# Performance work log

Hardware: AMD Instinct MI355X
Metric: run time of the kernel (lower is better)

The kernel has to match this reference:

```python
import jax, jax.numpy as jnp
import numpy as np


def setup_inputs() -> dict:
    key = jax.random.key(0)
    k1, k2, k3 = jax.random.split(key, 3)
    shape = (2, 16, 2048, 64)  # (b, num_heads, seq_len, d_k)
    Q = jax.random.normal(k1, shape, dtype=jnp.float32)
    K = jax.random.normal(k2, shape, dtype=jnp.float32)
    V = jax.random.normal(k3, shape, dtype=jnp.float32)
    return {"Q": Q, "K": K, "V": V}


def reference(Q, K, V):
    # Mathematically identical to the blockwise online-softmax loop:
    # causal softmax attention with scale 1/sqrt(d_k), plus logsumexp L.
    d_k = Q.shape[-1]
    seq_len = Q.shape[2]
    scale = 1.0 / np.sqrt(d_k).astype(np.float32)
    # scores: [b, h, q, k]
    S = jnp.einsum("bhqd,bhkd->bhqk", Q, K) * scale
    causal_mask = jnp.tril(jnp.ones((seq_len, seq_len), dtype=bool))  # k_pos <= q_pos
    S = jnp.where(causal_mask, S, -jnp.inf)
    # L_i = m_i + log(l_i) == logsumexp over key dim (every row has >=1 valid key)
    L = jax.nn.logsumexp(S, axis=-1, keepdims=True)  # [b, h, q, 1]
    P = jnp.exp(S - L)  # normalized probabilities (deferred-normalization result)
    O = jnp.einsum("bhqk,bhkd->bhqd", P, V)
    return O, L
```

## Files before the change

### kernel.cpp

```cpp
#include <hip/hip_runtime.h>
#include <hip/hip_bf16.h>

#define S_LEN 2048
#define DH    64
#define NBH   32
#define KSCALE 0.1803368801111f
#define LN2    0.6931471805599453f
#define MB2    4.0f

typedef short v4s __attribute__((ext_vector_type(4)));
typedef short v8s __attribute__((ext_vector_type(8)));
typedef float v4f __attribute__((ext_vector_type(4)));

__device__ __forceinline__ unsigned short f2bf(float f){
  union { float f; unsigned int u; } v; v.f = f;
  return (unsigned short)((v.u + 0x7FFFu + ((v.u >> 16) & 1u)) >> 16);
}

__device__ __forceinline__ void gld16(void* lds, const void* g){
  __builtin_amdgcn_global_load_lds(
      (const __attribute__((address_space(1))) unsigned int*)g,
      (__attribute__((address_space(3))) unsigned int*)lds, 16, 0, 0);
}

__global__ __launch_bounds__(256) void prep(const float* __restrict__ K,
                                            const float* __restrict__ V,
                                            unsigned short* __restrict__ Kf,
                                            unsigned short* __restrict__ Vf){
  __shared__ unsigned short s[64 * 72];
  const int t   = blockIdx.x;
  const int bh  = blockIdx.y;
  const int tid = threadIdx.x;

  const float* Ksrc = K + ((size_t)bh * S_LEN + t * 64) * DH;
  #pragma unroll
  for (int i = 0; i < 4; ++i){
    int f = tid + i * 256;
    float4 v = ((const float4*)Ksrc)[f];
    int row = f >> 4, col = (f & 15) * 4;
    ushort4 o; o.x = f2bf(v.x); o.y = f2bf(v.y); o.z = f2bf(v.z); o.w = f2bf(v.w);
    *(ushort4*)(&s[row * 72 + col]) = o;
  }
  __syncthreads();
  unsigned short* KfT = Kf + ((size_t)bh * 32 + t) * 4096;
  #pragma unroll
  for (int i = 0; i < 2; ++i){
    int item = tid + i * 256;
    int c = item >> 6, l = item & 63;
    int kb = c >> 1, h = c & 1;
    v8s frag = *(const v8s*)(&s[(kb * 16 + (l & 15)) * 72 + h * 32 + (l >> 4) * 8]);
    *(v8s*)(&KfT[c * 512 + l * 8]) = frag;
  }
  __syncthreads();

  const float* Vsrc = V + ((size_t)bh * S_LEN + t * 64) * DH;
  #pragma unroll
  for (int i = 0; i < 4; ++i){
    int f = tid + i * 256;
    float4 v = ((const float4*)Vsrc)[f];
    int k = f >> 4, d = (f & 15) * 4;
    s[(d + 0) * 72 + k] = f2bf(v.x);
    s[(d + 1) * 72 + k] = f2bf(v.y);
    s[(d + 2) * 72 + k] = f2bf(v.z);
    s[(d + 3) * 72 + k] = f2bf(v.w);
  }
  __syncthreads();
  unsigned short* VfT = Vf + ((size_t)bh * 32 + t) * 4096;
  #pragma unroll
  for (int i = 0; i < 2; ++i){
    int item = tid + i * 256;
    int c = item >> 6, l = item & 63;
    int db = c >> 1, kp = c & 1;
    int dd = db * 16 + (l & 15);
    int kk = kp * 32 + (l >> 4) * 4;
    v4s a = *(const v4s*)(&s[dd * 72 + kk]);
    v4s b = *(const v4s*)(&s[dd * 72 + kk + 16]);
    v8s fr; fr[0]=a[0]; fr[1]=a[1]; fr[2]=a[2]; fr[3]=a[3];
            fr[4]=b[0]; fr[5]=b[1]; fr[6]=b[2]; fr[7]=b[3];
    *(v8s*)(&VfT[c * 512 + l * 8]) = fr;
  }
}

__global__ __launch_bounds__(256, 3) void fa_fwd(
    const float* __restrict__ Q,
    const unsigned short* __restrict__ Kf,
    const unsigned short* __restrict__ Vf,
    float* __restrict__ O, float* __restrict__ L)
{
  __shared__ __align__(16) char smem[2][16384];

  const int tid  = threadIdx.x;
  const int w    = tid >> 6;
  const int lane = tid & 63;
  const int lq   = lane & 15;
  const int g    = lane >> 4;
  const int bid  = blockIdx.x;
  const int qt   = 31 - (bid >> 5);
  const int bh   = bid & 31;
  const int M    = qt + 1;

  const unsigned short* KfB = Kf + (size_t)bh * 32 * 4096;
  const unsigned short* VfB = Vf + (size_t)bh * 32 * 4096;

  auto issue = [&](int t, char* buf){
    #pragma unroll
    for (int i = 0; i < 2; ++i){
      const int slot = tid + i * 256;
      gld16(buf        + slot * 16, KfB + (size_t)t * 4096 + slot * 8);
      gld16(buf + 8192 + slot * 16, VfB + (size_t)t * 4096 + slot * 8);
    }
  };

  v8s qf[4][2];
  #pragma unroll
  for (int s = 0; s < 4; ++s){
    const float* qp = Q + (size_t)(bh * S_LEN + qt * 64 + s * 16 + lq) * DH + g * 8;
    #pragma unroll
    for (int h = 0; h < 2; ++h){
      float4 a = *(const float4*)(qp + h * 32);
      float4 b = *(const float4*)(qp + h * 32 + 4);
      v8s qv;
      qv[0]=(short)f2bf(a.x*KSCALE); qv[1]=(short)f2bf(a.y*KSCALE);
      qv[2]=(short)f2bf(a.z*KSCALE); qv[3]=(short)f2bf(a.w*KSCALE);
      qv[4]=(short)f2bf(b.x*KSCALE); qv[5]=(short)f2bf(b.y*KSCALE);
      qv[6]=(short)f2bf(b.z*KSCALE); qv[7]=(short)f2bf(b.w*KSCALE);
      qf[s][h] = qv;
    }
  }

  issue(0, smem[0]);

  const v4f zero  = {0.f, 0.f, 0.f, 0.f};
  const v4f minit = {-MB2, -MB2, -MB2, -MB2};
  v4f acc[4][4];
  #pragma unroll
  for (int s = 0; s < 4; ++s)
    #pragma unroll
    for (int db = 0; db < 4; ++db) acc[s][db] = zero;
  float l4[4] = {0.f, 0.f, 0.f, 0.f};

  const int kb    = w;
  const int koff0 = (kb * 2    ) * 1024 + lane * 16;
  const int koff1 = (kb * 2 + 1) * 1024 + lane * 16;
  const int vsub  = (kb >> 1) * 1024 + (kb & 1) * 8 + lane * 16;

  for (int t = 0; t < M; ++t){
    const int tn = (t + 1 < M) ? t + 1 : t;
    issue(tn, smem[(t + 1) & 1]);
    asm volatile("s_waitcnt vmcnt(4)" ::: "memory");
    __builtin_amdgcn_s_barrier();
    __builtin_amdgcn_sched_barrier(0);

    const char* kbase = smem[t & 1];
    const char* vbase = smem[t & 1] + 8192;

    v8s kf0 = *(const v8s*)(kbase + koff0);
    v8s kf1 = *(const v8s*)(kbase + koff1);
    v4s vv[4];
    #pragma unroll
    for (int db = 0; db < 4; ++db)
      vv[db] = *(const v4s*)(vbase + db * 2048 + vsub);

    float p4[4][4];
    __builtin_amdgcn_s_setprio(1);
    #pragma unroll
    for (int s = 0; s < 4; ++s){
      v4f st = minit;
      st = __builtin_amdgcn_mfma_f32_16x16x32_bf16(kf0, qf[s][0], st, 0, 0, 0);
      st = __builtin_amdgcn_mfma_f32_16x16x32_bf16(kf1, qf[s][1], st, 0, 0, 0);
      p4[s][0] = st[0]; p4[s][1] = st[1]; p4[s][2] = st[2]; p4[s][3] = st[3];
    }
    __builtin_amdgcn_s_setprio(0);

    if (t == qt){
      #pragma unroll
      for (int s = 0; s < 4; ++s)
        #pragma unroll
        for (int r = 0; r < 4; ++r)
          if (kb * 16 + g * 4 + r > s * 16 + lq) p4[s][r] = -INFINITY;
    }

    v4s pf[4];
    #pragma unroll
    for (int s = 0; s < 4; ++s){
      #pragma unroll
      for (int r = 0; r < 4; ++r){
        const float pe = __builtin_amdgcn_exp2f(p4[s][r]);
        p4[s][r] = pe;
        l4[s] += pe;
      }
      unsigned u0, u1;
      asm("v_cvt_pk_bf16_f32 %0, %1, %2" : "=v"(u0) : "v"(p4[s][0]), "v"(p4[s][1]));
      asm("v_cvt_pk_bf16_f32 %0, %1, %2" : "=v"(u1) : "v"(p4[s][2]), "v"(p4[s][3]));
      union { unsigned u[2]; v4s s4; } P; P.u[0] = u0; P.u[1] = u1;
      pf[s] = P.s4;
    }

    __builtin_amdgcn_s_setprio(1);
    #pragma unroll
    for (int s = 0; s < 4; ++s){
      acc[s][0] = __builtin_amdgcn_mfma_f32_16x16x16bf16_1k(vv[0], pf[s], acc[s][0], 0, 0, 0);
      acc[s][1] = __builtin_amdgcn_mfma_f32_16x16x16bf16_1k(vv[1], pf[s], acc[s][1], 0, 0, 0);
      acc[s][2] = __builtin_amdgcn_mfma_f32_16x16x16bf16_1k(vv[2], pf[s], acc[s][2], 0, 0, 0);
      acc[s][3] = __builtin_amdgcn_mfma_f32_16x16x16bf16_1k(vv[3], pf[s], acc[s][3], 0, 0, 0);
    }
    __builtin_amdgcn_s_setprio(0);
    __builtin_amdgcn_s_barrier();
    __builtin_amdgcn_sched_barrier(0);
  }

  asm volatile("s_waitcnt vmcnt(0)" ::: "memory");
  __builtin_amdgcn_sched_barrier(0);
  __syncthreads();

  #pragma unroll
  for (int s = 0; s < 4; ++s){
    l4[s] += __shfl_xor(l4[s], 16);
    l4[s] += __shfl_xor(l4[s], 32);
  }
  float* Lr = (float*)smem[1];
  if (lane < 16){
    #pragma unroll
    for (int s = 0; s < 4; ++s) Lr[(w * 4 + s) * 16 + lane] = l4[s];
  }
  __syncthreads();
  const float lfw = Lr[(0 * 4 + w) * 16 + lq] + Lr[(1 * 4 + w) * 16 + lq]
                  + Lr[(2 * 4 + w) * 16 + lq] + Lr[(3 * 4 + w) * 16 + lq];
  const float invw = 1.f / lfw;

  v4f* Or = (v4f*)smem[0];
  float* Ob = O + ((size_t)bh * S_LEN + qt * 64 + w * 16 + lq) * DH;
  #pragma unroll
  for (int db = 0; db < 4; ++db){
    __syncthreads();
    #pragma unroll
    for (int s = 0; s < 4; ++s) Or[((w * 4 + s) * 16 + lq) * 4 + g] = acc[s][db];
    __syncthreads();
    v4f o = Or[((0 * 4 + w) * 16 + lq) * 4 + g] + Or[((1 * 4 + w) * 16 + lq) * 4 + g]
          + Or[((2 * 4 + w) * 16 + lq) * 4 + g] + Or[((3 * 4 + w) * 16 + lq) * 4 + g];
    o *= invw;
    *(v4f*)(Ob + db * 16 + g * 4) = o;
  }
  if (lane < 16)
    L[(size_t)bh * S_LEN + qt * 64 + w * 16 + lane] = logf(lfw) + MB2 * LN2;
}

__global__ __launch_bounds__(64) void fa_naive(
    const float* __restrict__ Q, const float* __restrict__ K,
    const float* __restrict__ V, float* __restrict__ O, float* __restrict__ L)
{
  const int q  = blockIdx.x;
  const int bh = blockIdx.y;
  const int d  = threadIdx.x;
  const float qv = Q[(size_t)(bh * S_LEN + q) * DH + d];
  float m = -INFINITY, l = 0.f, o = 0.f;
  for (int k = 0; k <= q; ++k){
    float s = qv * K[(size_t)(bh * S_LEN + k) * DH + d];
    #pragma unroll
    for (int off = 32; off > 0; off >>= 1) s += __shfl_xor(s, off);
    s *= 0.125f;
    const float mn = fmaxf(m, s);
    const float sfc = expf(m - mn);
    const float pe = expf(s - mn);
    l = l * sfc + pe;
    o = o * sfc + pe * V[(size_t)(bh * S_LEN + k) * DH + d];
    m = mn;
  }
  O[(size_t)(bh * S_LEN + q) * DH + d] = o / l;
  if (d == 0) L[(size_t)bh * S_LEN + q] = m + logf(l);
}

extern "C" void kernel_launch(void* const* d_in, const int* in_sizes, int n_in,
                              void* d_out, int out_size, void* d_ws, size_t ws_size,
                              hipStream_t stream)
{
  (void)in_sizes; (void)n_in; (void)out_size;
  const float* Q = (const float*)d_in[0];
  const float* K = (const float*)d_in[1];
  const float* V = (const float*)d_in[2];
  float* O = (float*)d_out;
  float* L = O + (size_t)NBH * S_LEN * DH;

  const size_t half = (size_t)NBH * S_LEN * DH * sizeof(unsigned short);
  if (ws_size >= 2 * half){
    unsigned short* Kf = (unsigned short*)d_ws;
    unsigned short* Vf = Kf + (size_t)NBH * S_LEN * DH;
    prep<<<dim3(S_LEN / 64, NBH), 256, 0, stream>>>(K, V, Kf, Vf);
    fa_fwd<<<dim3(1024), 256, 0, stream>>>(Q, Kf, Vf, O, L);
  } else {
    fa_naive<<<dim3(S_LEN, NBH), 64, 0, stream>>>(Q, K, V, O, L);
  }
}
```

Measured before the change: 48.82 us.

## Repack V fragments for 16-byte LDS reads, reorder tiles, raise occupancy

The V pre-pack kernel now stores fragments so each wave reads its V operands with two 16-byte LDS loads instead of four 8-byte loads, matching the K access pattern. The q-tile schedule changes from strict longest-first to a serpentine order within groups of eight tiles, which changes how causal work is balanced across CUs. Launch bounds now request four blocks per SM instead of three, which caps registers per thread more tightly and may cause spills. A local variable is renamed to avoid shadowing.

```diff
diff --git a/kernel.cpp b/kernel.cpp
--- a/kernel.cpp
+++ b/kernel.cpp
@@ -70,18 +70,17 @@
   for (int i = 0; i < 2; ++i){
     int item = tid + i * 256;
     int c = item >> 6, l = item & 63;
-    int db = c >> 1, kp = c & 1;
-    int dd = db * 16 + (l & 15);
-    int kk = kp * 32 + (l >> 4) * 4;
-    v4s a = *(const v4s*)(&s[dd * 72 + kk]);
-    v4s b = *(const v4s*)(&s[dd * 72 + kk + 16]);
+    int kb = c >> 1, dp = c & 1;
+    int kk = kb * 16 + (l >> 4) * 4;
+    v4s a = *(const v4s*)(&s[((dp * 2 + 0) * 16 + (l & 15)) * 72 + kk]);
+    v4s b = *(const v4s*)(&s[((dp * 2 + 1) * 16 + (l & 15)) * 72 + kk]);
     v8s fr; fr[0]=a[0]; fr[1]=a[1]; fr[2]=a[2]; fr[3]=a[3];
             fr[4]=b[0]; fr[5]=b[1]; fr[6]=b[2]; fr[7]=b[3];
     *(v8s*)(&VfT[c * 512 + l * 8]) = fr;
   }
 }
 
-__global__ __launch_bounds__(256, 3) void fa_fwd(
+__global__ __launch_bounds__(256, 4) void fa_fwd(
     const float* __restrict__ Q,
     const unsigned short* __restrict__ Kf,
     const unsigned short* __restrict__ Vf,
@@ -95,7 +94,9 @@
   const int lq   = lane & 15;
   const int g    = lane >> 4;
   const int bid  = blockIdx.x;
-  const int qt   = 31 - (bid >> 5);
+  const int o    = bid >> 5;
+  const int hi   = o >> 3, lo = o & 7;
+  const int qt   = hi * 8 + ((hi & 1) ? (7 - lo) : lo);
   const int bh   = bid & 31;
   const int M    = qt + 1;
 
@@ -142,7 +143,8 @@
   const int kb    = w;
   const int koff0 = (kb * 2    ) * 1024 + lane * 16;
   const int koff1 = (kb * 2 + 1) * 1024 + lane * 16;
-  const int vsub  = (kb >> 1) * 1024 + (kb & 1) * 8 + lane * 16;
+  const int voff0 = (kb * 2    ) * 1024 + lane * 16;
+  const int voff1 = (kb * 2 + 1) * 1024 + lane * 16;
 
   for (int t = 0; t < M; ++t){
     const int tn = (t + 1 < M) ? t + 1 : t;
@@ -156,10 +158,10 @@
 
     v8s kf0 = *(const v8s*)(kbase + koff0);
     v8s kf1 = *(const v8s*)(kbase + koff1);
-    v4s vv[4];
-    #pragma unroll
-    for (int db = 0; db < 4; ++db)
-      vv[db] = *(const v4s*)(vbase + db * 2048 + vsub);
+    v8s vv0 = *(const v8s*)(vbase + voff0);
+    v8s vv1 = *(const v8s*)(vbase + voff1);
+    v4s vv[4] = { {vv0[0],vv0[1],vv0[2],vv0[3]}, {vv0[4],vv0[5],vv0[6],vv0[7]},
+                  {vv1[0],vv1[1],vv1[2],vv1[3]}, {vv1[4],vv1[5],vv1[6],vv1[7]} };
 
     float p4[4][4];
     __builtin_amdgcn_s_setprio(1);
@@ -236,10 +238,10 @@
     #pragma unroll
     for (int s = 0; s < 4; ++s) Or[((w * 4 + s) * 16 + lq) * 4 + g] = acc[s][db];
     __syncthreads();
-    v4f o = Or[((0 * 4 + w) * 16 + lq) * 4 + g] + Or[((1 * 4 + w) * 16 + lq) * 4 + g]
-          + Or[((2 * 4 + w) * 16 + lq) * 4 + g] + Or[((3 * 4 + w) * 16 + lq) * 4 + g];
-    o *= invw;
-    *(v4f*)(Ob + db * 16 + g * 4) = o;
+    v4f o2 = Or[((0 * 4 + w) * 16 + lq) * 4 + g] + Or[((1 * 4 + w) * 16 + lq) * 4 + g]
+           + Or[((2 * 4 + w) * 16 + lq) * 4 + g] + Or[((3 * 4 + w) * 16 + lq) * 4 + g];
+    o2 *= invw;
+    *(v4f*)(Ob + db * 16 + g * 4) = o2;
   }
   if (lane < 16)
     L[(size_t)bh * S_LEN + qt * 64 + w * 16 + lane] = logf(lfw) + MB2 * LN2;
```

Result: slower. 75.92 us (+55.5%).
